# Kernel optimization log

Measured on AMD Instinct MI355X. Metric: run time of the kernel, lower is better.

## Reference

```python
import jax, jax.numpy as jnp
import numpy as np

DIM = 512
N_LAYERS = 2
N_HEADS = 8
HEAD_DIM = DIM // N_HEADS
VOCAB = 50257
MAX_SEQ = 2048
N_LEVELS = 3  # len(chunk_sizes)
HID = 4 * DIM
B, S = 2, 1024
STD = 0.02
EPS = 1e-5


def setup_inputs() -> dict:
    key = jax.random.key(0)
    ks = jax.random.split(key, 12)
    f32 = jnp.float32
    inp = {}
    inp["input_ids"] = jax.random.randint(ks[0], (B, S), 0, VOCAB)
    inp["tok_emb"] = jax.random.normal(ks[1], (VOCAB, DIM), f32) * STD  # tied with head
    inp["pos_emb"] = jax.random.normal(ks[2], (MAX_SEQ, DIM), f32) * STD
    # attention projections, stored [in, out] so y = x @ W (math-equivalent to torch x @ W.T)
    inp["Wq"] = jax.random.normal(ks[3], (N_LAYERS, DIM, DIM), f32) * STD
    inp["Wk"] = jax.random.normal(ks[4], (N_LAYERS, DIM, DIM), f32) * STD
    inp["Wv"] = jax.random.normal(ks[5], (N_LAYERS, DIM, DIM), f32) * STD
    inp["Wo"] = jax.random.normal(ks[6], (N_LAYERS, DIM, DIM), f32) * STD
    # layer norms
    inp["ln1_g"] = jnp.ones((N_LAYERS, DIM), f32)
    inp["ln1_b"] = jnp.zeros((N_LAYERS, DIM), f32)
    inp["ln2_g"] = jnp.ones((N_LAYERS, DIM), f32)
    inp["ln2_b"] = jnp.zeros((N_LAYERS, DIM), f32)
    inp["lnf_g"] = jnp.ones((DIM,), f32)
    inp["lnf_b"] = jnp.zeros((DIM,), f32)
    # continuum memory system: N_LEVELS chained MLPs per layer
    inp["W1"] = jax.random.normal(ks[7], (N_LAYERS, N_LEVELS, DIM, HID), f32) * STD
    inp["b1"] = jnp.zeros((N_LAYERS, N_LEVELS, HID), f32)
    inp["W2"] = jax.random.normal(ks[8], (N_LAYERS, N_LEVELS, HID, DIM), f32) * STD
    inp["b2"] = jnp.zeros((N_LAYERS, N_LEVELS, DIM), f32)
    return inp


def layer_norm(x, g, b):
    mu = jnp.mean(x, axis=-1, keepdims=True)
    var = jnp.var(x, axis=-1, keepdims=True)
    return (x - mu) / jnp.sqrt(var + EPS) * g + b


def linear_attention_with_memory(x, Wq, Wk, Wv, Wo):
    # x: [B, S, D]. Fast-weight recurrence: M_t = M_{t-1} + v_t k_t^T ; y_t = M_t q_t
    Bsz, Slen, D = x.shape
    H, hd = N_HEADS, HEAD_DIM

    def proj(W):  # -> [S, B, H, hd] (time-major for scan)
        return jnp.moveaxis((x @ W).reshape(Bsz, Slen, H, hd), 1, 0)

    q, k, v = proj(Wq), proj(Wk), proj(Wv)
    M0 = jnp.zeros((Bsz, H, hd, hd), x.dtype)

    def step(M, qkv):
        q_t, k_t, v_t = qkv
        M = M + jnp.einsum('bhd,bhk->bhdk', v_t, k_t)
        y_t = jnp.einsum('bhdk,bhk->bhd', M, q_t)
        return M, y_t

    _, ys = jax.lax.scan(step, M0, (q, k, v))  # ys: [S, B, H, hd]
    y = jnp.moveaxis(ys, 0, 1).reshape(Bsz, Slen, D)
    return y @ Wo


def cms(x, W1, b1, W2, b2):
    # chained MLP levels (dropout=0 / eval mode)
    for m in range(W1.shape[0]):
        x = jax.nn.gelu(x @ W1[m] + b1[m]) @ W2[m] + b2[m]
    return x


def reference(input_ids, tok_emb, pos_emb, Wq, Wk, Wv, Wo,
              ln1_g, ln1_b, ln2_g, ln2_b, lnf_g, lnf_b,
              W1, b1, W2, b2):
    Bsz, Slen = input_ids.shape
    x = tok_emb[input_ids] + pos_emb[:Slen][None, :, :]
    for l in range(Wq.shape[0]):
        x = x + linear_attention_with_memory(layer_norm(x, ln1_g[l], ln1_b[l]),
                                             Wq[l], Wk[l], Wv[l], Wo[l])
        x = x + cms(layer_norm(x, ln2_g[l], ln2_b[l]), W1[l], b1[l], W2[l], b2[l])
    x = layer_norm(x, lnf_g, lnf_b)
    logits = x @ tok_emb.T  # tied head
    return logits
```

## Files before the change

### kernel.cpp

```cpp
#include <hip/hip_runtime.h>
#include <hip/hip_bf16.h>
#include <cstdint>

using bf16 = __hip_bfloat16;
typedef __attribute__((ext_vector_type(8))) __bf16 bf16x8;
typedef __attribute__((ext_vector_type(4))) float f32x4;
typedef __attribute__((ext_vector_type(4))) unsigned int u32x4;

#define SEQ    1024
#define BATCH  2
#define ROWS   (BATCH*SEQ)
#define DMODEL 512
#define HIDDEN 2048
#define NHEADS 8
#define HD     64
#define VOCABN 50257
#define CHUNK  32
#define NCHUNK (SEQ/CHUNK)
#define QKVW   1536

__device__ __forceinline__ float gelu_tanh(float x) {
  float u = 0.7978845608028654f * (x + 0.044715f * x * x * x);
  return 0.5f * x * (1.0f + tanhf(u));
}

__global__ __launch_bounds__(512, 2)
void head_sb(const bf16* __restrict__ A, const bf16* __restrict__ Bt,
             float* __restrict__ C, int N)
{
  __shared__ __align__(16) bf16 As[128 * 64];
  __shared__ __align__(16) bf16 Bs[256 * 64];
  const int t = threadIdx.x, lane = t & 63;
  const int w = t >> 6, wm = w >> 2, wn = w & 3;
  const int tm = blockIdx.x & 15, tn = blockIdx.x >> 4;
  const int arow0 = tm * 128, brow0 = tn * 256;
  const int rA = lane & 15;
  const int ko0 = lane >> 4;

  f32x4 acc[4][4];
#pragma unroll
  for (int m = 0; m < 4; ++m)
#pragma unroll
    for (int n = 0; n < 4; ++n) acc[m][n] = (f32x4){0.f, 0.f, 0.f, 0.f};

  for (int k0 = 0; k0 < 512; k0 += 64) {
#pragma unroll
    for (int rep = 0; rep < 2; ++rep) {
      int c = rep * 512 + t;
      int row = c >> 3, ko = c & 7;
      const bf16* ga = A + (size_t)(arow0 + row) * 512 + k0 + (ko ^ (row & 7)) * 8;
      __builtin_amdgcn_global_load_lds(
          (const __attribute__((address_space(1))) unsigned int*)ga,
          (__attribute__((address_space(3))) unsigned int*)(As + row * 64 + ko * 8),
          16, 0, 0);
    }
#pragma unroll
    for (int rep = 0; rep < 4; ++rep) {
      int c = rep * 512 + t;
      int row = c >> 3, ko = c & 7;
      int br = brow0 + row; br = br < N ? br : N - 1;
      const bf16* gb = Bt + (size_t)br * 512 + k0 + (ko ^ (row & 7)) * 8;
      __builtin_amdgcn_global_load_lds(
          (const __attribute__((address_space(1))) unsigned int*)gb,
          (__attribute__((address_space(3))) unsigned int*)(Bs + row * 64 + ko * 8),
          16, 0, 0);
    }
    asm volatile("s_waitcnt vmcnt(0)" ::: "memory");
    __syncthreads();

    {
      bf16x8 af[4], bfv[4];
#pragma unroll
      for (int fm = 0; fm < 4; ++fm) {
        int row = wm * 64 + fm * 16 + rA;
        af[fm] = __builtin_bit_cast(bf16x8,
            *(const u32x4*)((const char*)As + row * 128 + ((ko0 ^ (row & 7)) << 4)));
      }
#pragma unroll
      for (int fn = 0; fn < 4; ++fn) {
        int row = wn * 64 + fn * 16 + rA;
        bfv[fn] = __builtin_bit_cast(bf16x8,
            *(const u32x4*)((const char*)Bs + row * 128 + ((ko0 ^ (row & 7)) << 4)));
      }
#pragma unroll
      for (int fm = 0; fm < 4; ++fm)
#pragma unroll
        for (int fn = 0; fn < 4; ++fn)
          acc[fm][fn] = __builtin_amdgcn_mfma_f32_16x16x32_bf16(af[fm], bfv[fn], acc[fm][fn], 0, 0, 0);
    }
    {
      bf16x8 af[4], bfv[4];
#pragma unroll
      for (int fm = 0; fm < 4; ++fm) {
        int row = wm * 64 + fm * 16 + rA;
        af[fm] = __builtin_bit_cast(bf16x8,
            *(const u32x4*)((const char*)As + row * 128 + (((ko0 ^ (row & 7)) << 4) ^ 64)));
      }
#pragma unroll
      for (int fn = 0; fn < 4; ++fn) {
        int row = wn * 64 + fn * 16 + rA;
        bfv[fn] = __builtin_bit_cast(bf16x8,
            *(const u32x4*)((const char*)Bs + row * 128 + (((ko0 ^ (row & 7)) << 4) ^ 64)));
      }
#pragma unroll
      for (int fm = 0; fm < 4; ++fm)
#pragma unroll
        for (int fn = 0; fn < 4; ++fn)
          acc[fm][fn] = __builtin_amdgcn_mfma_f32_16x16x32_bf16(af[fm], bfv[fn], acc[fm][fn], 0, 0, 0);
    }
    __syncthreads();
  }

#pragma unroll
  for (int fm = 0; fm < 4; ++fm) {
    const int row = arow0 + wm * 64 + fm * 16 + (lane >> 4) * 4;
#pragma unroll
    for (int fn = 0; fn < 4; ++fn) {
      const int col = brow0 + wn * 64 + fn * 16 + rA;
      if (col < N) {
#pragma unroll
        for (int r = 0; r < 4; ++r)
          C[(size_t)(row + r) * N + col] = acc[fm][fn][r];
      }
    }
  }
}

template<int EPI>
__global__ __launch_bounds__(256, 4)
void gemm_mid(const bf16* __restrict__ A, const bf16* __restrict__ Bt,
              void* __restrict__ Cout, const float* __restrict__ bias,
              int M, int N, int K, int Ks, int ldc, int ntn)
{
  __shared__ __align__(16) bf16 As[128 * 64];
  __shared__ __align__(16) bf16 Bs[64 * 64];
  const int t = threadIdx.x;
  const int lane = t & 63;
  const int w = t >> 6;
  const int wr = w >> 1, wc = w & 1;
  const int tm = blockIdx.x / ntn, tn = blockIdx.x % ntn;
  const int sk = blockIdx.y;
  const int kbeg = sk * Ks;
  const int rA = lane & 15;
  const int ko0 = lane >> 4;

  f32x4 acc[4][2];
#pragma unroll
  for (int m = 0; m < 4; ++m)
#pragma unroll
    for (int n = 0; n < 2; ++n) acc[m][n] = (f32x4){0.f, 0.f, 0.f, 0.f};

  for (int k0 = kbeg; k0 < kbeg + Ks; k0 += 64) {
#pragma unroll
    for (int rep = 0; rep < 4; ++rep) {
      int c = rep * 256 + t;
      int row = c >> 3, ko = c & 7;
      const bf16* ga = A + (size_t)(tm * 128 + row) * K + k0 + (ko ^ (row & 7)) * 8;
      __builtin_amdgcn_global_load_lds(
          (const __attribute__((address_space(1))) unsigned int*)ga,
          (__attribute__((address_space(3))) unsigned int*)(As + row * 64 + ko * 8),
          16, 0, 0);
    }
#pragma unroll
    for (int rep = 0; rep < 2; ++rep) {
      int c = rep * 256 + t;
      int row = c >> 3, ko = c & 7;
      const bf16* gb = Bt + (size_t)(tn * 64 + row) * K + k0 + (ko ^ (row & 7)) * 8;
      __builtin_amdgcn_global_load_lds(
          (const __attribute__((address_space(1))) unsigned int*)gb,
          (__attribute__((address_space(3))) unsigned int*)(Bs + row * 64 + ko * 8),
          16, 0, 0);
    }
    asm volatile("s_waitcnt vmcnt(0)" ::: "memory");
    __syncthreads();

    {
      bf16x8 af[4], bfv[2];
#pragma unroll
      for (int m = 0; m < 4; ++m) {
        int row = wr * 64 + m * 16 + rA;
        af[m] = __builtin_bit_cast(bf16x8,
            *(const u32x4*)((const char*)As + row * 128 + ((ko0 ^ (row & 7)) << 4)));
      }
#pragma unroll
      for (int n = 0; n < 2; ++n) {
        int row = wc * 32 + n * 16 + rA;
        bfv[n] = __builtin_bit_cast(bf16x8,
            *(const u32x4*)((const char*)Bs + row * 128 + ((ko0 ^ (row & 7)) << 4)));
      }
#pragma unroll
      for (int m = 0; m < 4; ++m)
#pragma unroll
        for (int n = 0; n < 2; ++n)
          acc[m][n] = __builtin_amdgcn_mfma_f32_16x16x32_bf16(af[m], bfv[n], acc[m][n], 0, 0, 0);
    }
    {
      bf16x8 af[4], bfv[2];
#pragma unroll
      for (int m = 0; m < 4; ++m) {
        int row = wr * 64 + m * 16 + rA;
        af[m] = __builtin_bit_cast(bf16x8,
            *(const u32x4*)((const char*)As + row * 128 + (((ko0 ^ (row & 7)) << 4) ^ 64)));
      }
#pragma unroll
      for (int n = 0; n < 2; ++n) {
        int row = wc * 32 + n * 16 + rA;
        bfv[n] = __builtin_bit_cast(bf16x8,
            *(const u32x4*)((const char*)Bs + row * 128 + (((ko0 ^ (row & 7)) << 4) ^ 64)));
      }
#pragma unroll
      for (int m = 0; m < 4; ++m)
#pragma unroll
        for (int n = 0; n < 2; ++n)
          acc[m][n] = __builtin_amdgcn_mfma_f32_16x16x32_bf16(af[m], bfv[n], acc[m][n], 0, 0, 0);
    }
    __syncthreads();
  }

#pragma unroll
  for (int m = 0; m < 4; ++m) {
    const int row = tm * 128 + wr * 64 + m * 16 + (lane >> 4) * 4;
#pragma unroll
    for (int n = 0; n < 2; ++n) {
      const int col = tn * 64 + wc * 32 + n * 16 + rA;
#pragma unroll
      for (int r = 0; r < 4; ++r) {
        float v = acc[m][n][r];
        if (EPI == 0) {
          ((float*)Cout)[(size_t)(row + r) * ldc + col] = v;
        } else if (EPI == 1) {
          ((float*)Cout)[(size_t)sk * M * N + (size_t)(row + r) * N + col] = v;
        } else {
          v += bias[col]; v = gelu_tanh(v);
          ((bf16*)Cout)[(size_t)(row + r) * ldc + col] = __float2bfloat16(v);
        }
      }
    }
  }
}

__global__ __launch_bounds__(256)
void reduce_bias_bf16(const float* __restrict__ part, bf16* __restrict__ out,
                      const float* __restrict__ bias)
{
  int i = blockIdx.x * 256 + threadIdx.x;
  const float4* p4 = (const float4*)part;
  const size_t str = (size_t)ROWS * DMODEL / 4;
  float4 v = p4[i];
  float4 v1 = p4[i + str], v2 = p4[i + 2 * str], v3 = p4[i + 3 * str];
  v.x += v1.x + v2.x + v3.x; v.y += v1.y + v2.y + v3.y;
  v.z += v1.z + v2.z + v3.z; v.w += v1.w + v2.w + v3.w;
  float4 bb = ((const float4*)bias)[i & (DMODEL / 4 - 1)];
  v.x += bb.x; v.y += bb.y; v.z += bb.z; v.w += bb.w;
  union { bf16 h[4]; uint2 u; } cv;
  cv.h[0] = __float2bfloat16(v.x); cv.h[1] = __float2bfloat16(v.y);
  cv.h[2] = __float2bfloat16(v.z); cv.h[3] = __float2bfloat16(v.w);
  ((uint2*)out)[i] = cv.u;
}

template<bool BIAS>
__global__ __launch_bounds__(256)
void reduce_resid_ln(const float* __restrict__ part, float* __restrict__ x,
                     const float* __restrict__ bias, const float* __restrict__ g,
                     const float* __restrict__ b, bf16* __restrict__ xn)
{
  int lane = threadIdx.x & 63;
  int row = blockIdx.x * 4 + (threadIdx.x >> 6);
  const float4* p4 = (const float4*)part;
  const size_t str = (size_t)ROWS * DMODEL / 4;
  size_t base = (size_t)row * (DMODEL / 4) + lane * 2;
  float4 a0 = p4[base], a1 = p4[base + 1];
#pragma unroll
  for (int s = 1; s < 4; ++s) {
    float4 q0 = p4[base + s * str], q1 = p4[base + 1 + s * str];
    a0.x += q0.x; a0.y += q0.y; a0.z += q0.z; a0.w += q0.w;
    a1.x += q1.x; a1.y += q1.y; a1.z += q1.z; a1.w += q1.w;
  }
  if (BIAS) {
    float4 b0 = ((const float4*)bias)[lane * 2];
    float4 b1 = ((const float4*)bias)[lane * 2 + 1];
    a0.x += b0.x; a0.y += b0.y; a0.z += b0.z; a0.w += b0.w;
    a1.x += b1.x; a1.y += b1.y; a1.z += b1.z; a1.w += b1.w;
  }
  float4* xr = (float4*)(x + (size_t)row * DMODEL);
  float4 x0 = xr[lane * 2], x1 = xr[lane * 2 + 1];
  x0.x += a0.x; x0.y += a0.y; x0.z += a0.z; x0.w += a0.w;
  x1.x += a1.x; x1.y += a1.y; x1.z += a1.z; x1.w += a1.w;
  xr[lane * 2] = x0; xr[lane * 2 + 1] = x1;
  float s  = x0.x + x0.y + x0.z + x0.w + x1.x + x1.y + x1.z + x1.w;
  float ss = x0.x*x0.x + x0.y*x0.y + x0.z*x0.z + x0.w*x0.w
           + x1.x*x1.x + x1.y*x1.y + x1.z*x1.z + x1.w*x1.w;
#pragma unroll
  for (int off = 32; off > 0; off >>= 1) { s += __shfl_xor(s, off); ss += __shfl_xor(ss, off); }
  float mu = s * (1.f / DMODEL);
  float inv = rsqrtf(ss * (1.f / DMODEL) - mu * mu + 1e-5f);
  int c0 = lane * 8;
  float vv[8] = {x0.x, x0.y, x0.z, x0.w, x1.x, x1.y, x1.z, x1.w};
#pragma unroll
  for (int j = 0; j < 8; ++j)
    xn[(size_t)row * DMODEL + c0 + j] = __float2bfloat16((vv[j] - mu) * inv * g[c0 + j] + b[c0 + j]);
}

__global__ __launch_bounds__(256)
void embed_ln(const int* __restrict__ ids, const float* __restrict__ te,
              const float* __restrict__ pe, const float* __restrict__ g,
              const float* __restrict__ b, float* __restrict__ x, bf16* __restrict__ xn)
{
  int lane = threadIdx.x & 63;
  int row = blockIdx.x * 4 + (threadIdx.x >> 6);
  int sq = row & (SEQ - 1);
  int id = ids[row];
  const float4* tr = (const float4*)(te + (size_t)id * DMODEL);
  const float4* pr = (const float4*)(pe + (size_t)sq * DMODEL);
  float4 x0 = tr[lane * 2], x1 = tr[lane * 2 + 1];
  float4 p0 = pr[lane * 2], p1 = pr[lane * 2 + 1];
  x0.x += p0.x; x0.y += p0.y; x0.z += p0.z; x0.w += p0.w;
  x1.x += p1.x; x1.y += p1.y; x1.z += p1.z; x1.w += p1.w;
  float4* xr = (float4*)(x + (size_t)row * DMODEL);
  xr[lane * 2] = x0; xr[lane * 2 + 1] = x1;
  float s  = x0.x + x0.y + x0.z + x0.w + x1.x + x1.y + x1.z + x1.w;
  float ss = x0.x*x0.x + x0.y*x0.y + x0.z*x0.z + x0.w*x0.w
           + x1.x*x1.x + x1.y*x1.y + x1.z*x1.z + x1.w*x1.w;
#pragma unroll
  for (int off = 32; off > 0; off >>= 1) { s += __shfl_xor(s, off); ss += __shfl_xor(ss, off); }
  float mu = s * (1.f / DMODEL);
  float inv = rsqrtf(ss * (1.f / DMODEL) - mu * mu + 1e-5f);
  int c0 = lane * 8;
  float vv[8] = {x0.x, x0.y, x0.z, x0.w, x1.x, x1.y, x1.z, x1.w};
#pragma unroll
  for (int j = 0; j < 8; ++j)
    xn[(size_t)row * DMODEL + c0 + j] = __float2bfloat16((vv[j] - mu) * inv * g[c0 + j] + b[c0 + j]);
}

__global__ __launch_bounds__(256)
void transpose_cvt(const float* __restrict__ in, bf16* __restrict__ out, int R, int C)
{
  __shared__ float tile[32][33];
  int mat = blockIdx.z;
  const float* src = in + (size_t)mat * R * C;
  bf16* dst = out + (size_t)mat * R * C;
  int c0 = blockIdx.x * 32, r0 = blockIdx.y * 32;
  int tx = threadIdx.x, ty = threadIdx.y;
#pragma unroll
  for (int i = ty; i < 32; i += 8)
    tile[i][tx] = src[(size_t)(r0 + i) * C + c0 + tx];
  __syncthreads();
#pragma unroll
  for (int i = ty; i < 32; i += 8)
    dst[(size_t)(c0 + i) * R + r0 + tx] = __float2bfloat16(tile[tx][i]);
}

__global__ __launch_bounds__(256)
void transpose_qkv(const float* __restrict__ Wq, const float* __restrict__ Wk,
                   const float* __restrict__ Wv, bf16* __restrict__ out)
{
  __shared__ float tile[32][33];
  int z = blockIdx.z;
  int l = z / 3, p = z % 3;
  const float* src = (p == 0 ? Wq : (p == 1 ? Wk : Wv)) + (size_t)l * DMODEL * DMODEL;
  bf16* dst = out + (size_t)l * QKVW * DMODEL + (size_t)p * DMODEL * DMODEL;
  int c0 = blockIdx.x * 32, r0 = blockIdx.y * 32;
  int tx = threadIdx.x, ty = threadIdx.y;
#pragma unroll
  for (int i = ty; i < 32; i += 8)
    tile[i][tx] = src[(size_t)(r0 + i) * DMODEL + c0 + tx];
  __syncthreads();
#pragma unroll
  for (int i = ty; i < 32; i += 8)
    dst[(size_t)(c0 + i) * DMODEL + r0 + tx] = __float2bfloat16(tile[tx][i]);
}

__global__ void cvt_bf16_k(const float* __restrict__ in, bf16* __restrict__ out, int n4)
{
  int i = blockIdx.x * 256 + threadIdx.x;
  if (i >= n4) return;
  float4 v = ((const float4*)in)[i];
  union { bf16 h[4]; uint2 u; } cv;
  cv.h[0] = __float2bfloat16(v.x); cv.h[1] = __float2bfloat16(v.y);
  cv.h[2] = __float2bfloat16(v.z); cv.h[3] = __float2bfloat16(v.w);
  ((uint2*)out)[i] = cv.u;
}

__global__ __launch_bounds__(256)
void scan_ktv(const float* __restrict__ qkv, float* __restrict__ ktv)
{
  int blk = blockIdx.x;
  int c = blk & (NCHUNK - 1), bh = blk >> 5;
  int b = bh >> 3, h = bh & 7;
  __shared__ float ks[CHUNK][64], vs[CHUNK][64];
  int t = threadIdx.x;
  size_t base = ((size_t)(b * SEQ + c * CHUNK)) * QKVW + h * HD;
#pragma unroll
  for (int i = 0; i < CHUNK * 64 / 256; ++i) {
    int idx = i * 256 + t;
    int s = idx >> 6, e = idx & 63;
    ks[s][e] = qkv[base + 512 + (size_t)s * QKVW + e];
    vs[s][e] = qkv[base + 1024 + (size_t)s * QKVW + e];
  }
  __syncthreads();
  int e = t >> 2, d0 = (t & 3) * 16;
  float acc[16];
#pragma unroll
  for (int j = 0; j < 16; ++j) acc[j] = 0.f;
  for (int s = 0; s < CHUNK; ++s) {
    float kv = ks[s][e];
#pragma unroll
    for (int j = 0; j < 16; ++j) acc[j] += kv * vs[s][d0 + j];
  }
  float* o = ktv + (size_t)blk * 4096 + e * 64 + d0;
#pragma unroll
  for (int j = 0; j < 16; ++j) o[j] = acc[j];
}

__global__ __launch_bounds__(256)
void scan_attn(const float* __restrict__ qkv, const float* __restrict__ ktv,
               bf16* __restrict__ y)
{
  int blk = blockIdx.x;
  int c = blk & (NCHUNK - 1), bh = blk >> 5;
  int b = bh >> 3, h = bh & 7;
  __shared__ float qs[CHUNK][65], ks[CHUNK][65], vs[CHUNK][65];
  __shared__ float Ss[CHUNK][CHUNK + 1];
  __shared__ float Ms[64][65];
  int t = threadIdx.x;
  size_t base = ((size_t)(b * SEQ + c * CHUNK)) * QKVW + h * HD;
#pragma unroll
  for (int i = 0; i < CHUNK * 64 / 256; ++i) {
    int idx = i * 256 + t;
    int s = idx >> 6, e = idx & 63;
    qs[s][e] = qkv[base + (size_t)s * QKVW + e];
    ks[s][e] = qkv[base + 512 + (size_t)s * QKVW + e];
    vs[s][e] = qkv[base + 1024 + (size_t)s * QKVW + e];
  }
  {
    int e = t >> 2, d0 = (t & 3) * 16;
    float mp[16];
#pragma unroll
    for (int j = 0; j < 16; ++j) mp[j] = 0.f;
    for (int cp = 0; cp < c; ++cp) {
      const float* p = ktv + ((size_t)bh * NCHUNK + cp) * 4096 + e * 64 + d0;
#pragma unroll
      for (int j = 0; j < 16; ++j) mp[j] += p[j];
    }
#pragma unroll
    for (int j = 0; j < 16; ++j) Ms[e][d0 + j] = mp[j];
  }
  __syncthreads();
  {
    int si = t >> 3, j0 = (t & 7) * 4;
    float sa[4] = {0.f, 0.f, 0.f, 0.f};
    for (int e = 0; e < 64; ++e) {
      float qv = qs[si][e];
#pragma unroll
      for (int j = 0; j < 4; ++j) sa[j] += qv * ks[j0 + j][e];
    }
#pragma unroll
    for (int j = 0; j < 4; ++j) Ss[si][j0 + j] = (j0 + j <= si) ? sa[j] : 0.f;
  }
  __syncthreads();
  {
    int si = t >> 3, d0 = (t & 7) * 8;
    float ya[8];
#pragma unroll
    for (int j = 0; j < 8; ++j) ya[j] = 0.f;
    for (int sp = 0; sp < CHUNK; ++sp) {
      float sv = Ss[si][sp];
#pragma unroll
      for (int j = 0; j < 8; ++j) ya[j] += sv * vs[sp][d0 + j];
    }
    for (int e = 0; e < 64; ++e) {
      float qv = qs[si][e];
#pragma unroll
      for (int j = 0; j < 8; ++j) ya[j] += qv * Ms[e][d0 + j];
    }
    bf16* o = y + ((size_t)(b * SEQ + c * CHUNK + si)) * DMODEL + h * HD + d0;
#pragma unroll
    for (int j = 0; j < 8; ++j) o[j] = __float2bfloat16(ya[j]);
  }
}

extern "C" void kernel_launch(void* const* d_in, const int* in_sizes, int n_in,
                              void* d_out, int out_size, void* d_ws, size_t ws_size,
                              hipStream_t stream)
{
  const int*   ids  = (const int*)  d_in[0];
  const float* tok  = (const float*)d_in[1];
  const float* pos  = (const float*)d_in[2];
  const float* Wq   = (const float*)d_in[3];
  const float* Wk   = (const float*)d_in[4];
  const float* Wv   = (const float*)d_in[5];
  const float* Wo   = (const float*)d_in[6];
  const float* ln1g = (const float*)d_in[7];
  const float* ln1b = (const float*)d_in[8];
  const float* ln2g = (const float*)d_in[9];
  const float* ln2b = (const float*)d_in[10];
  const float* lnfg = (const float*)d_in[11];
  const float* lnfb = (const float*)d_in[12];
  const float* W1   = (const float*)d_in[13];
  const float* b1   = (const float*)d_in[14];
  const float* W2   = (const float*)d_in[15];
  const float* b2   = (const float*)d_in[16];
  float* out = (float*)d_out;

  char* ws = (char*)d_ws;
  size_t off = 0;
  auto alloc = [&](size_t bytes) { void* p = ws + off; off += (bytes + 255) & ~(size_t)255; return p; };
  bf16* QKVt = (bf16*)alloc((size_t)2 * QKVW * 512 * 2);
  bf16* Wot  = (bf16*)alloc((size_t)2 * 512 * 512 * 2);
  bf16* W1t  = (bf16*)alloc((size_t)6 * 512 * 2048 * 2);
  bf16* W2t  = (bf16*)alloc((size_t)6 * 2048 * 512 * 2);
  bf16* tokb = (bf16*)alloc((size_t)VOCABN * 512 * 2);
  float* x   = (float*)alloc((size_t)ROWS * 512 * 4);
  bf16*  xn  = (bf16*) alloc((size_t)ROWS * 512 * 2);
  bf16*  tbuf= (bf16*) alloc((size_t)ROWS * 512 * 2);
  bf16*  hbuf= (bf16*) alloc((size_t)ROWS * 2048 * 2);
  float* qkvf= (float*)alloc((size_t)ROWS * QKVW * 4);
  bf16*  yb  = (bf16*) alloc((size_t)ROWS * 512 * 2);
  float* ktv = (float*)alloc((size_t)16 * NCHUNK * 4096 * 4);
  float* part= (float*)alloc((size_t)4 * ROWS * 512 * 4);

  dim3 tb(32, 8);
  transpose_qkv<<<dim3(16, 16, 6), tb, 0, stream>>>(Wq, Wk, Wv, QKVt);
  transpose_cvt<<<dim3(16, 16, 2), tb, 0, stream>>>(Wo, Wot, 512, 512);
  transpose_cvt<<<dim3(64, 16, 6), tb, 0, stream>>>(W1, W1t, 512, 2048);
  transpose_cvt<<<dim3(16, 64, 6), tb, 0, stream>>>(W2, W2t, 2048, 512);
  int n4 = VOCABN * 512 / 4;
  cvt_bf16_k<<<(n4 + 255) / 256, 256, 0, stream>>>(tok, tokb, n4);

  embed_ln<<<ROWS / 4, 256, 0, stream>>>(ids, tok, pos, ln1g, ln1b, x, xn);

  for (int l = 0; l < 2; ++l) {
    gemm_mid<0><<<dim3(16 * (QKVW / 64)), 256, 0, stream>>>(
        xn, QKVt + (size_t)l * QKVW * 512, qkvf, nullptr, ROWS, QKVW, 512, 512, QKVW, QKVW / 64);
    scan_ktv<<<16 * NCHUNK, 256, 0, stream>>>(qkvf, ktv);
    scan_attn<<<16 * NCHUNK, 256, 0, stream>>>(qkvf, ktv, yb);
    gemm_mid<1><<<dim3(16 * 8, 4), 256, 0, stream>>>(
        yb, Wot + (size_t)l * 512 * 512, part, nullptr, ROWS, 512, 512, 128, 512, 8);
    reduce_resid_ln<false><<<ROWS / 4, 256, 0, stream>>>(
        part, x, nullptr, ln2g + l * 512, ln2b + l * 512, xn);

    const bf16* cur = xn;
    for (int m = 0; m < 3; ++m) {
      int lm = l * 3 + m;
      gemm_mid<2><<<dim3(16 * (2048 / 64)), 256, 0, stream>>>(
          cur, W1t + (size_t)lm * 2048 * 512, hbuf, b1 + (size_t)lm * 2048,
          ROWS, 2048, 512, 512, 2048, 2048 / 64);
      gemm_mid<1><<<dim3(16 * 8, 4), 256, 0, stream>>>(
          hbuf, W2t + (size_t)lm * 512 * 2048, part, nullptr, ROWS, 512, 2048, 512, 512, 8);
      if (m < 2) {
        reduce_bias_bf16<<<ROWS * 512 / 4 / 256, 256, 0, stream>>>(part, tbuf, b2 + (size_t)lm * 512);
        cur = tbuf;
      } else {
        const float* g = (l == 0) ? (ln1g + 512) : lnfg;
        const float* b = (l == 0) ? (ln1b + 512) : lnfb;
        reduce_resid_ln<true><<<ROWS / 4, 256, 0, stream>>>(part, x, b2 + (size_t)lm * 512, g, b, xn);
      }
    }
  }

  int ntn_h = (VOCABN + 255) / 256;
  head_sb<<<dim3(16 * ntn_h), 512, 0, stream>>>(xn, tokb, out, VOCABN);
}
```

Before: 603.8 us.

## Replace LDS-staged LM head GEMM with direct global-to-register MFMA loads

The tied-head GEMM no longer stages A and B tiles through shared memory with barriers. Each wave loads its MFMA fragments straight from global memory, and the block tile shrinks to 64x256 with four waves splitting the N dimension. The aim is to drop LDS traffic and synchronisation and to raise occupancy. The cost is uncoalesced 16-byte loads per lane and less on-chip reuse, so the kernel leans on L1/L2 to serve repeated A rows across waves.

```diff
diff --git a/kernel.cpp b/kernel.cpp
--- a/kernel.cpp
+++ b/kernel.cpp
@@ -24,18 +24,28 @@
   return 0.5f * x * (1.0f + tanhf(u));
 }
 
-__global__ __launch_bounds__(512, 2)
-void head_sb(const bf16* __restrict__ A, const bf16* __restrict__ Bt,
-             float* __restrict__ C, int N)
-{
-  __shared__ __align__(16) bf16 As[128 * 64];
-  __shared__ __align__(16) bf16 Bs[256 * 64];
+__global__ __launch_bounds__(256, 3)
+void head_direct(const bf16* __restrict__ A, const bf16* __restrict__ Bt,
+                 float* __restrict__ C, int N)
+{
   const int t = threadIdx.x, lane = t & 63;
-  const int w = t >> 6, wm = w >> 2, wn = w & 3;
-  const int tm = blockIdx.x & 15, tn = blockIdx.x >> 4;
-  const int arow0 = tm * 128, brow0 = tn * 256;
+  const int w = t >> 6;
+  const int tm = blockIdx.x & 31, tn = blockIdx.x >> 5;
+  const int arow0 = tm * 64;
+  const int bcol0 = tn * 256 + w * 64;
   const int rA = lane & 15;
-  const int ko0 = lane >> 4;
+  const int ko = (lane >> 4) * 8;
+
+  const bf16* ap[4];
+  const bf16* bp[4];
+#pragma unroll
+  for (int fm = 0; fm < 4; ++fm)
+    ap[fm] = A + (size_t)(arow0 + fm * 16 + rA) * 512 + ko;
+#pragma unroll
+  for (int fn = 0; fn < 4; ++fn) {
+    int br = bcol0 + fn * 16 + rA; br = br < N ? br : N - 1;
+    bp[fn] = Bt + (size_t)br * 512 + ko;
+  }
 
   f32x4 acc[4][4];
 #pragma unroll
@@ -43,80 +53,28 @@
 #pragma unroll
     for (int n = 0; n < 4; ++n) acc[m][n] = (f32x4){0.f, 0.f, 0.f, 0.f};
 
-  for (int k0 = 0; k0 < 512; k0 += 64) {
-#pragma unroll
-    for (int rep = 0; rep < 2; ++rep) {
-      int c = rep * 512 + t;
-      int row = c >> 3, ko = c & 7;
-      const bf16* ga = A + (size_t)(arow0 + row) * 512 + k0 + (ko ^ (row & 7)) * 8;
-      __builtin_amdgcn_global_load_lds(
-          (const __attribute__((address_space(1))) unsigned int*)ga,
-          (__attribute__((address_space(3))) unsigned int*)(As + row * 64 + ko * 8),
-          16, 0, 0);
-    }
-#pragma unroll
-    for (int rep = 0; rep < 4; ++rep) {
-      int c = rep * 512 + t;
-      int row = c >> 3, ko = c & 7;
-      int br = brow0 + row; br = br < N ? br : N - 1;
-      const bf16* gb = Bt + (size_t)br * 512 + k0 + (ko ^ (row & 7)) * 8;
-      __builtin_amdgcn_global_load_lds(
-          (const __attribute__((address_space(1))) unsigned int*)gb,
-          (__attribute__((address_space(3))) unsigned int*)(Bs + row * 64 + ko * 8),
-          16, 0, 0);
-    }
-    asm volatile("s_waitcnt vmcnt(0)" ::: "memory");
-    __syncthreads();
-
-    {
-      bf16x8 af[4], bfv[4];
-#pragma unroll
-      for (int fm = 0; fm < 4; ++fm) {
-        int row = wm * 64 + fm * 16 + rA;
-        af[fm] = __builtin_bit_cast(bf16x8,
-            *(const u32x4*)((const char*)As + row * 128 + ((ko0 ^ (row & 7)) << 4)));
-      }
-#pragma unroll
-      for (int fn = 0; fn < 4; ++fn) {
-        int row = wn * 64 + fn * 16 + rA;
-        bfv[fn] = __builtin_bit_cast(bf16x8,
-            *(const u32x4*)((const char*)Bs + row * 128 + ((ko0 ^ (row & 7)) << 4)));
-      }
-#pragma unroll
-      for (int fm = 0; fm < 4; ++fm)
-#pragma unroll
-        for (int fn = 0; fn < 4; ++fn)
-          acc[fm][fn] = __builtin_amdgcn_mfma_f32_16x16x32_bf16(af[fm], bfv[fn], acc[fm][fn], 0, 0, 0);
-    }
-    {
-      bf16x8 af[4], bfv[4];
-#pragma unroll
-      for (int fm = 0; fm < 4; ++fm) {
-        int row = wm * 64 + fm * 16 + rA;
-        af[fm] = __builtin_bit_cast(bf16x8,
-            *(const u32x4*)((const char*)As + row * 128 + (((ko0 ^ (row & 7)) << 4) ^ 64)));
-      }
-#pragma unroll
-      for (int fn = 0; fn < 4; ++fn) {
-        int row = wn * 64 + fn * 16 + rA;
-        bfv[fn] = __builtin_bit_cast(bf16x8,
-            *(const u32x4*)((const char*)Bs + row * 128 + (((ko0 ^ (row & 7)) << 4) ^ 64)));
-      }
-#pragma unroll
-      for (int fm = 0; fm < 4; ++fm)
-#pragma unroll
-        for (int fn = 0; fn < 4; ++fn)
-          acc[fm][fn] = __builtin_amdgcn_mfma_f32_16x16x32_bf16(af[fm], bfv[fn], acc[fm][fn], 0, 0, 0);
-    }
-    __syncthreads();
+#pragma unroll 2
+  for (int k0 = 0; k0 < 512; k0 += 32) {
+    bf16x8 af[4], bfv[4];
+#pragma unroll
+    for (int fm = 0; fm < 4; ++fm)
+      af[fm] = __builtin_bit_cast(bf16x8, *(const u32x4*)(ap[fm] + k0));
+#pragma unroll
+    for (int fn = 0; fn < 4; ++fn)
+      bfv[fn] = __builtin_bit_cast(bf16x8, *(const u32x4*)(bp[fn] + k0));
+#pragma unroll
+    for (int fm = 0; fm < 4; ++fm)
+#pragma unroll
+      for (int fn = 0; fn < 4; ++fn)
+        acc[fm][fn] = __builtin_amdgcn_mfma_f32_16x16x32_bf16(af[fm], bfv[fn], acc[fm][fn], 0, 0, 0);
   }
 
 #pragma unroll
   for (int fm = 0; fm < 4; ++fm) {
-    const int row = arow0 + wm * 64 + fm * 16 + (lane >> 4) * 4;
+    const int row = arow0 + fm * 16 + (lane >> 4) * 4;
 #pragma unroll
     for (int fn = 0; fn < 4; ++fn) {
-      const int col = brow0 + wn * 64 + fn * 16 + rA;
+      const int col = bcol0 + fn * 16 + rA;
       if (col < N) {
 #pragma unroll
         for (int r = 0; r < 4; ++r)
@@ -559,5 +517,5 @@
   }
 
   int ntn_h = (VOCABN + 255) / 256;
-  head_sb<<<dim3(16 * ntn_h), 512, 0, stream>>>(xn, tokb, out, VOCABN);
-}
+  head_direct<<<dim3(32 * ntn_h), 256, 0, stream>>>(xn, tokb, out, VOCABN);
+}
```

Result: slower. 821.6 us (+36.1%).
